# Kernel tuning notes

Hardware: AMD Instinct MI355X
Metric: run time of the kernel (lower is better)

Reference implementation:

```python
import jax, jax.numpy as jnp
import numpy as np


def _patch_indices():
    # 36 positions (6x6 grid), each gathering a 3x3 window of 6-channel squares
    # from the flattened 385-vector: index = x*48 + y*6 + c
    idx = []
    for i in range(36):
        x, y = i // 6, i % 6
        rows = []
        for ox in range(3):
            for oy in range(3):
                base = (x + ox) * 48 + (y + oy) * 6
                rows.extend(range(base, base + 6))
        idx.append(rows)
    return jnp.asarray(np.array(idx, dtype=np.int32))  # [36, 54]


_IDX = _patch_indices()


def _crelu(v):
    return jnp.clip(v, -1.0, 1.0)


def setup_inputs() -> dict:
    key = jax.random.key(0)
    ks = jax.random.split(key, 13)
    B = 131072
    inp = jax.random.normal(ks[0], (B, 385), dtype=jnp.float32)
    s = 0.2  # small init scale
    # sight stack: 54 -> 8 -> 8 -> 1  (stored as [in, out])
    W1 = jax.random.normal(ks[1], (54, 8), jnp.float32) * s
    b1 = jax.random.normal(ks[2], (8,), jnp.float32) * s
    W2 = jax.random.normal(ks[3], (8, 8), jnp.float32) * s
    b2 = jax.random.normal(ks[4], (8,), jnp.float32) * s
    W3 = jax.random.normal(ks[5], (8, 1), jnp.float32) * s
    b3 = jax.random.normal(ks[6], (1,), jnp.float32) * s
    # evaluation stack: 37 -> 16 -> 16 -> 1
    E1 = jax.random.normal(ks[7], (37, 16), jnp.float32) * s
    c1 = jax.random.normal(ks[8], (16,), jnp.float32) * s
    E2 = jax.random.normal(ks[9], (16, 16), jnp.float32) * s
    c2 = jax.random.normal(ks[10], (16,), jnp.float32) * s
    E3 = jax.random.normal(ks[11], (16, 1), jnp.float32) * s
    c3 = jax.random.normal(ks[12], (1,), jnp.float32) * s
    return {"inp": inp, "W1": W1, "b1": b1, "W2": W2, "b2": b2,
            "W3": W3, "b3": b3, "E1": E1, "c1": c1, "E2": E2, "c2": c2,
            "E3": E3, "c3": c3}


def reference(inp, W1, b1, W2, b2, W3, b3, E1, c1, E2, c2, E3, c3):
    # inp: [B, 385]
    patches = inp[:, _IDX]                       # [B, 36, 54] windowed gather
    h = _crelu(jnp.einsum('bpf,fo->bpo', patches, W1) + b1)   # [B, 36, 8]
    h = _crelu(jnp.einsum('bpf,fo->bpo', h, W2) + b2)         # [B, 36, 8]
    v = _crelu(jnp.einsum('bpf,fo->bpo', h, W3) + b3)[..., 0]  # [B, 36]
    vision = jnp.concatenate([v, inp[:, 384:385]], axis=1)    # [B, 37]
    g = _crelu(vision @ E1 + c1)                 # [B, 16]
    g = _crelu(g @ E2 + c2)                      # [B, 16]
    out = _crelu(g @ E3 + c3)                    # [B, 1]
    return out
```

## Files before the change

kernel.cpp:

```cpp
#include <hip/hip_runtime.h>

typedef __attribute__((ext_vector_type(8))) short short8;
typedef __attribute__((ext_vector_type(4))) float float4v;

__device__ __forceinline__ float crelu(float v) {
    return fminf(1.0f, fmaxf(-1.0f, v));
}
__device__ __forceinline__ uint f2bf_u(float v) {
    uint u = __float_as_uint(v);
    u += 0x7fffu + ((u >> 16) & 1u);
    return u >> 16;
}
__device__ __forceinline__ ushort f2bf(float v) { return (ushort)f2bf_u(v); }
__device__ __forceinline__ float bf2f_lo(uint u) { return __uint_as_float(u << 16); }
__device__ __forceinline__ float bf2f_hi(uint u) { return __uint_as_float(u & 0xffff0000u); }
__device__ __forceinline__ uint cvt_pk_bf16(float a, float b) {
    uint r;
    asm("v_cvt_pk_bf16_f32 %0, %1, %2" : "=v"(r) : "v"(a), "v"(b));
    return r;
}

#define ROW 385
#define BT  16

#define SLAB_BYTES 6656
#define E1T_OFF 960
#define E2T_OFF 3776
#define E1T_LD  44

__global__ __launch_bounds__(256, 6)
void lila_wave(const float* __restrict__ inp,
               const float* __restrict__ W1, const float* __restrict__ b1,
               const float* __restrict__ W2, const float* __restrict__ b2,
               const float* __restrict__ W3, const float* __restrict__ b3,
               const float* __restrict__ E1, const float* __restrict__ c1,
               const float* __restrict__ E2, const float* __restrict__ c2,
               const float* __restrict__ E3, const float* __restrict__ c3,
               float* __restrict__ out)
{
    __shared__ __align__(16) char slab_all[4 * SLAB_BYTES];

    const int tid  = threadIdx.x;
    const int lane = tid & 63;
    const int wv   = tid >> 6;
    const int quad = lane >> 4;
    const int nn   = lane & 15;
    const int m0   = quad * 8;

    char*   slab  = slab_all + wv * SLAB_BYTES;
    ushort* board = (ushort*)slab;
    ushort* hbuf  = (ushort*)(slab + 4352);
    float*  vis   = (float*)slab;
    float*  g1    = (float*)(slab + 640);
    float*  e1t   = (float*)(slab + E1T_OFF);
    ushort* e2t   = (ushort*)(slab + E2T_OFF);

    const long long b0w = (long long)blockIdx.x * BT + wv * 4;

    short8 bfr[3];
    #pragma unroll
    for (int r = 0; r < 3; ++r) {
        #pragma unroll
        for (int j = 0; j < 8; ++j) {
            int k = m0 + j, oy = k >> 3, c = k & 7;
            float w = (oy < 3 && c < 6 && nn < 8)
                    ? W1[(r * 18 + oy * 6 + c) * 8 + nn] : 0.0f;
            bfr[r][j] = (short)f2bf(w);
        }
    }
    const float bias1 = (nn < 8) ? b1[nn] : 0.0f;

    const int r   = lane >> 4;
    const int c16 = lane & 15;
    const float* gr = inp + (b0w + r) * ROW;

    if (c16 < 4) {
        uint4 z = {0u, 0u, 0u, 0u};
        *(uint4*)(board + r * 544 + 512 + c16 * 8) = z;
    }
    #pragma unroll
    for (int u = 0; u < 4; ++u) {
        int cell = c16 + 16 * u;
        int g = cell * 6;
        float4 q0 = *(const float4*)(gr + g);
        float2 q1 = *(const float2*)(gr + g + 4);
        uint4 pk;
        pk.x = cvt_pk_bf16(q0.x, q0.y);
        pk.y = cvt_pk_bf16(q0.z, q0.w);
        pk.z = cvt_pk_bf16(q1.x, q1.y);
        pk.w = 0u;
        *(uint4*)(board + r * 544 + cell * 8) = pk;
    }
    const float cen = gr[384];

    asm volatile("" ::: "memory");

    #pragma unroll 3
    for (int t = 0; t < 9; ++t) {
        int ltask = t * 16 + nn;
        uint lb = (uint)ltask / 36u;
        uint p  = (uint)ltask - 36u * lb;
        uint x  = p / 6u;
        uint y  = p - 6u * x;
        const ushort* base = board + lb * 544 + x * 64 + 8 * y + m0;
        union { uint4 u; short8 s; } a0, a1, a2;
        a0.u = *(const uint4*)(base);
        a1.u = *(const uint4*)(base + 64);
        a2.u = *(const uint4*)(base + 128);
        float4v acc = { bias1, bias1, bias1, bias1 };
        acc = __builtin_amdgcn_mfma_f32_16x16x32_bf16(a0.s, bfr[0], acc, 0, 0, 0);
        acc = __builtin_amdgcn_mfma_f32_16x16x32_bf16(a1.s, bfr[1], acc, 0, 0, 0);
        acc = __builtin_amdgcn_mfma_f32_16x16x32_bf16(a2.s, bfr[2], acc, 0, 0, 0);
        if (nn < 8) {
            uint w01 = cvt_pk_bf16(crelu(acc[0]), crelu(acc[1]));
            uint w23 = cvt_pk_bf16(crelu(acc[2]), crelu(acc[3]));
            ushort* hb = hbuf + (t * 16 + quad * 4) * 8 + nn;
            hb[0]  = (ushort)w01;
            hb[8]  = (ushort)(w01 >> 16);
            hb[16] = (ushort)w23;
            hb[24] = (ushort)(w23 >> 16);
        }
    }

    asm volatile("" ::: "memory");

    {
        float e1g[10];
        #pragma unroll
        for (int k = 0; k < 9; ++k) e1g[k] = E1[lane + 64 * k];
        if (lane < 16) e1g[9] = E1[lane + 576];
        float e2g[4];
        #pragma unroll
        for (int k = 0; k < 4; ++k) e2g[k] = E2[lane + 64 * k];

        #pragma unroll
        for (int k = 0; k < 9; ++k) e1t[nn * E1T_LD + r + 4 * k] = e1g[k];
        if (lane < 16) e1t[nn * E1T_LD + 36] = e1g[9];
        #pragma unroll
        for (int k = 0; k < 4; ++k) e2t[nn * 16 + r + 4 * k] = f2bf(e2g[k]);
    }
    const float c1v = c1[nn];
    const float c2v = c2[nn];
    const float e3v = E3[nn];

    asm volatile("" ::: "memory");

    {
        short8 w2fh, w2fl;
        const int colq = nn - quad * 8;
        #pragma unroll
        for (int j = 0; j < 8; ++j) {
            float w = (quad < 2 && colq >= 0 && colq < 8) ? W2[j * 8 + colq] : 0.0f;
            uint hb = f2bf_u(w);
            float wr = w - __uint_as_float(hb << 16);
            w2fh[j] = (short)hb;
            w2fl[j] = (short)f2bf(wr);
        }
        const float b2v = b2[nn & 7];
        const float w3v = W3[nn & 7];
        const float b3v = b3[0];

        #pragma unroll
        for (int t = 0; t < 5; ++t) {
            union { uint4 u; short8 s; } av;
            av.u.x = 0u; av.u.y = 0u; av.u.z = 0u; av.u.w = 0u;
            int tsk = t * 16 + nn + (quad ? 80 : 0);
            if (quad < 2 && (t < 4 || quad == 0))
                av.u = *(const uint4*)(hbuf + tsk * 8);
            float4v acc = { b2v, b2v, b2v, b2v };
            acc = __builtin_amdgcn_mfma_f32_16x16x32_bf16(av.s, w2fh, acc, 0, 0, 0);
            acc = __builtin_amdgcn_mfma_f32_16x16x32_bf16(av.s, w2fl, acc, 0, 0, 0);
            float vsum[4];
            #pragma unroll
            for (int i = 0; i < 4; ++i) {
                float vv = crelu(acc[i]) * w3v;
                vv += __shfl_xor(vv, 1);
                vv += __shfl_xor(vv, 2);
                vv += __shfl_xor(vv, 4);
                vsum[i] = vv;
            }
            const bool isA = (nn == 0);
            if ((nn & 7) == 0 && (isA || t < 4)) {
                int task = (isA ? 0 : 80) + t * 16 + quad * 4;
                uint lb = (uint)task / 36u;
                uint p  = (uint)task - 36u * lb;
                float4 o4;
                o4.x = crelu(vsum[0] + b3v);
                o4.y = crelu(vsum[1] + b3v);
                o4.z = crelu(vsum[2] + b3v);
                o4.w = crelu(vsum[3] + b3v);
                *(float4*)(vis + lb * 40 + p) = o4;
            }
        }
    }

    asm volatile("" ::: "memory");

    {
        const int o = nn;
        float a = c1v;
        #pragma unroll
        for (int fi = 0; fi < 9; ++fi) {
            float4 vv = *(const float4*)(vis + r * 40 + fi * 4);
            float4 ev = *(const float4*)(e1t + o * E1T_LD + fi * 4);
            a = fmaf(vv.x, ev.x, a);
            a = fmaf(vv.y, ev.y, a);
            a = fmaf(vv.z, ev.z, a);
            a = fmaf(vv.w, ev.w, a);
        }
        a = fmaf(cen, e1t[o * E1T_LD + 36], a);
        g1[r * 20 + o] = crelu(a);

        asm volatile("" ::: "memory");

        uint4 e2a = *(const uint4*)(e2t + o * 16);
        uint4 e2b = *(const uint4*)(e2t + o * 16 + 8);
        float a2 = c2v;
        #pragma unroll
        for (int fi = 0; fi < 4; ++fi) {
            float4 gv = *(const float4*)(g1 + r * 20 + fi * 4);
            uint w01 = (fi < 2) ? (fi == 0 ? e2a.x : e2a.z) : (fi == 2 ? e2b.x : e2b.z);
            uint w23 = (fi < 2) ? (fi == 0 ? e2a.y : e2a.w) : (fi == 2 ? e2b.y : e2b.w);
            a2 = fmaf(gv.x, bf2f_lo(w01), a2);
            a2 = fmaf(gv.y, bf2f_hi(w01), a2);
            a2 = fmaf(gv.z, bf2f_lo(w23), a2);
            a2 = fmaf(gv.w, bf2f_hi(w23), a2);
        }
        float tv = crelu(a2) * e3v;
        tv += __shfl_xor(tv, 1);
        tv += __shfl_xor(tv, 2);
        tv += __shfl_xor(tv, 4);
        tv += __shfl_xor(tv, 8);
        if (o == 0) out[b0w + r] = crelu(tv + c3[0]);
    }
}

extern "C" void kernel_launch(void* const* d_in, const int* in_sizes, int n_in,
                              void* d_out, int out_size, void* d_ws, size_t ws_size,
                              hipStream_t stream)
{
    const float* inp = (const float*)d_in[0];
    const float* W1  = (const float*)d_in[1];
    const float* b1  = (const float*)d_in[2];
    const float* W2  = (const float*)d_in[3];
    const float* b2  = (const float*)d_in[4];
    const float* W3  = (const float*)d_in[5];
    const float* b3  = (const float*)d_in[6];
    const float* E1  = (const float*)d_in[7];
    const float* c1  = (const float*)d_in[8];
    const float* E2  = (const float*)d_in[9];
    const float* c2  = (const float*)d_in[10];
    const float* E3  = (const float*)d_in[11];
    const float* c3  = (const float*)d_in[12];
    float* out = (float*)d_out;

    int B = in_sizes[0] / ROW;
    int grid = B / BT;
    lila_wave<<<grid, 256, 0, stream>>>(inp, W1, b1, W2, b2, W3, b3,
                                        E1, c1, E2, c2, E3, c3, out);
}
```

Before: 293.9 us.

## Reuse sliding-window rows in layer-1 MFMA loop and hoist weight loads

Layer 1 now walks each column of the 6x6 grid along x with a rotating three-row register window. Each step loads one new LDS row instead of three, and the per-task divide and modulo index math goes away. Positions are split into a 4-column group and a 2-column group, with the hbuf write layout adjusted to match. The W2, bias and E-weight global loads move earlier so their latency overlaps the convolution, and the E1/E2 LDS stores are deferred until after layer 2. The cost is higher register pressure and more complex indexing.

```diff
diff --git a/kernel.cpp b/kernel.cpp
--- a/kernel.cpp
+++ b/kernel.cpp
@@ -59,16 +59,35 @@
 
     short8 bfr[3];
     #pragma unroll
-    for (int r = 0; r < 3; ++r) {
+    for (int rr = 0; rr < 3; ++rr) {
         #pragma unroll
         for (int j = 0; j < 8; ++j) {
             int k = m0 + j, oy = k >> 3, c = k & 7;
             float w = (oy < 3 && c < 6 && nn < 8)
-                    ? W1[(r * 18 + oy * 6 + c) * 8 + nn] : 0.0f;
-            bfr[r][j] = (short)f2bf(w);
+                    ? W1[(rr * 18 + oy * 6 + c) * 8 + nn] : 0.0f;
+            bfr[rr][j] = (short)f2bf(w);
         }
     }
     const float bias1 = (nn < 8) ? b1[nn] : 0.0f;
+
+    short8 w2fh, w2fl;
+    {
+        const int colq = nn - quad * 8;
+        #pragma unroll
+        for (int j = 0; j < 8; ++j) {
+            float w = (quad < 2 && colq >= 0 && colq < 8) ? W2[j * 8 + colq] : 0.0f;
+            uint hb2 = f2bf_u(w);
+            float wr = w - __uint_as_float(hb2 << 16);
+            w2fh[j] = (short)hb2;
+            w2fl[j] = (short)f2bf(wr);
+        }
+    }
+    const float b2v = b2[nn & 7];
+    const float w3v = W3[nn & 7];
+    const float b3v = b3[0];
+    const float c1v = c1[nn];
+    const float c2v = c2[nn];
+    const float e3v = E3[nn];
 
     const int r   = lane >> 4;
     const int c16 = lane & 15;
@@ -95,71 +114,66 @@
 
     asm volatile("" ::: "memory");
 
-    #pragma unroll 3
-    for (int t = 0; t < 9; ++t) {
-        int ltask = t * 16 + nn;
-        uint lb = (uint)ltask / 36u;
-        uint p  = (uint)ltask - 36u * lb;
-        uint x  = p / 6u;
-        uint y  = p - 6u * x;
-        const ushort* base = board + lb * 544 + x * 64 + 8 * y + m0;
-        union { uint4 u; short8 s; } a0, a1, a2;
-        a0.u = *(const uint4*)(base);
-        a1.u = *(const uint4*)(base + 64);
-        a2.u = *(const uint4*)(base + 128);
-        float4v acc = { bias1, bias1, bias1, bias1 };
-        acc = __builtin_amdgcn_mfma_f32_16x16x32_bf16(a0.s, bfr[0], acc, 0, 0, 0);
-        acc = __builtin_amdgcn_mfma_f32_16x16x32_bf16(a1.s, bfr[1], acc, 0, 0, 0);
-        acc = __builtin_amdgcn_mfma_f32_16x16x32_bf16(a2.s, bfr[2], acc, 0, 0, 0);
-        if (nn < 8) {
-            uint w01 = cvt_pk_bf16(crelu(acc[0]), crelu(acc[1]));
-            uint w23 = cvt_pk_bf16(crelu(acc[2]), crelu(acc[3]));
-            ushort* hb = hbuf + (t * 16 + quad * 4) * 8 + nn;
-            hb[0]  = (ushort)w01;
-            hb[8]  = (ushort)(w01 >> 16);
-            hb[16] = (ushort)w23;
-            hb[24] = (ushort)(w23 >> 16);
+    {
+        const int lb0 = nn >> 2, y0 = nn & 3;
+        const ushort* base = board + lb0 * 544 + 8 * y0 + m0;
+        union { uint4 u; short8 s; } rw[3];
+        rw[0].u = *(const uint4*)(base);
+        rw[1].u = *(const uint4*)(base + 64);
+        #pragma unroll
+        for (int x = 0; x < 6; ++x) {
+            rw[(x + 2) % 3].u = *(const uint4*)(base + (x + 2) * 64);
+            float4v acc = { bias1, bias1, bias1, bias1 };
+            acc = __builtin_amdgcn_mfma_f32_16x16x32_bf16(rw[x % 3].s,       bfr[0], acc, 0, 0, 0);
+            acc = __builtin_amdgcn_mfma_f32_16x16x32_bf16(rw[(x + 1) % 3].s, bfr[1], acc, 0, 0, 0);
+            acc = __builtin_amdgcn_mfma_f32_16x16x32_bf16(rw[(x + 2) % 3].s, bfr[2], acc, 0, 0, 0);
+            if (nn < 8) {
+                uint w01 = cvt_pk_bf16(crelu(acc[0]), crelu(acc[1]));
+                uint w23 = cvt_pk_bf16(crelu(acc[2]), crelu(acc[3]));
+                ushort* hb = hbuf + (quad * 36 + x * 6) * 8 + nn;
+                hb[0]  = (ushort)w01;
+                hb[8]  = (ushort)(w01 >> 16);
+                hb[16] = (ushort)w23;
+                hb[24] = (ushort)(w23 >> 16);
+            }
+        }
+    }
+    {
+        const int lb1 = (nn >> 1) & 3, y1 = 4 + (nn & 1);
+        const ushort* base = board + lb1 * 544 + 8 * y1 + m0;
+        union { uint4 u; short8 s; } rw[3];
+        rw[0].u = *(const uint4*)(base);
+        rw[1].u = *(const uint4*)(base + 64);
+        #pragma unroll
+        for (int x = 0; x < 6; ++x) {
+            rw[(x + 2) % 3].u = *(const uint4*)(base + (x + 2) * 64);
+            float4v acc = { bias1, bias1, bias1, bias1 };
+            acc = __builtin_amdgcn_mfma_f32_16x16x32_bf16(rw[x % 3].s,       bfr[0], acc, 0, 0, 0);
+            acc = __builtin_amdgcn_mfma_f32_16x16x32_bf16(rw[(x + 1) % 3].s, bfr[1], acc, 0, 0, 0);
+            acc = __builtin_amdgcn_mfma_f32_16x16x32_bf16(rw[(x + 2) % 3].s, bfr[2], acc, 0, 0, 0);
+            if (quad < 2 && nn < 8) {
+                uint w01 = cvt_pk_bf16(crelu(acc[0]), crelu(acc[1]));
+                uint w23 = cvt_pk_bf16(crelu(acc[2]), crelu(acc[3]));
+                ushort* hb = hbuf + ((2 * quad) * 36 + x * 6 + 4) * 8 + nn;
+                hb[0]   = (ushort)w01;
+                hb[8]   = (ushort)(w01 >> 16);
+                hb[288] = (ushort)w23;
+                hb[296] = (ushort)(w23 >> 16);
+            }
         }
     }
 
     asm volatile("" ::: "memory");
 
-    {
-        float e1g[10];
-        #pragma unroll
-        for (int k = 0; k < 9; ++k) e1g[k] = E1[lane + 64 * k];
-        if (lane < 16) e1g[9] = E1[lane + 576];
-        float e2g[4];
-        #pragma unroll
-        for (int k = 0; k < 4; ++k) e2g[k] = E2[lane + 64 * k];
-
-        #pragma unroll
-        for (int k = 0; k < 9; ++k) e1t[nn * E1T_LD + r + 4 * k] = e1g[k];
-        if (lane < 16) e1t[nn * E1T_LD + 36] = e1g[9];
-        #pragma unroll
-        for (int k = 0; k < 4; ++k) e2t[nn * 16 + r + 4 * k] = f2bf(e2g[k]);
-    }
-    const float c1v = c1[nn];
-    const float c2v = c2[nn];
-    const float e3v = E3[nn];
-
-    asm volatile("" ::: "memory");
-
-    {
-        short8 w2fh, w2fl;
-        const int colq = nn - quad * 8;
-        #pragma unroll
-        for (int j = 0; j < 8; ++j) {
-            float w = (quad < 2 && colq >= 0 && colq < 8) ? W2[j * 8 + colq] : 0.0f;
-            uint hb = f2bf_u(w);
-            float wr = w - __uint_as_float(hb << 16);
-            w2fh[j] = (short)hb;
-            w2fl[j] = (short)f2bf(wr);
-        }
-        const float b2v = b2[nn & 7];
-        const float w3v = W3[nn & 7];
-        const float b3v = b3[0];
-
+    float e1g[10];
+    #pragma unroll
+    for (int k = 0; k < 9; ++k) e1g[k] = E1[lane + 64 * k];
+    if (lane < 16) e1g[9] = E1[lane + 576];
+    float e2g[4];
+    #pragma unroll
+    for (int k = 0; k < 4; ++k) e2g[k] = E2[lane + 64 * k];
+
+    {
         #pragma unroll
         for (int t = 0; t < 5; ++t) {
             union { uint4 u; short8 s; } av;
@@ -193,6 +207,12 @@
             }
         }
     }
+
+    #pragma unroll
+    for (int k = 0; k < 9; ++k) e1t[nn * E1T_LD + r + 4 * k] = e1g[k];
+    if (lane < 16) e1t[nn * E1T_LD + 36] = e1g[9];
+    #pragma unroll
+    for (int k = 0; k < 4; ++k) e2t[nn * 16 + r + 4 * k] = f2bf(e2g[k]);
 
     asm volatile("" ::: "memory");
 
```

Result: no change. 295.8 us (+0.7%).

## Process two row groups per wave with register prefetch of next group

Applied to the files above, without the earlier changes.

Each wave now handles two groups of 4 rows instead of one, and the launch grid shrinks by half. The input rows for the next group are loaded into registers while the current group's layer-1 results are consumed, then packed into the board buffer after the current group finishes. The aim is to hide global load latency behind compute and to amortise weight setup across more rows. In exchange it costs extra registers, under a launch bound that already targets 6 blocks, and it halves the block count. The E1/E2 staging into shared memory is also moved inside the loop, so it repeats for every group.

```diff
diff --git a/kernel.cpp b/kernel.cpp
--- a/kernel.cpp
+++ b/kernel.cpp
@@ -21,7 +21,7 @@
 }
 
 #define ROW 385
-#define BT  16
+#define NG  2
 
 #define SLAB_BYTES 6656
 #define E1T_OFF 960
@@ -46,6 +46,8 @@
     const int quad = lane >> 4;
     const int nn   = lane & 15;
     const int m0   = quad * 8;
+    const int r    = lane >> 4;
+    const int c16  = lane & 15;
 
     char*   slab  = slab_all + wv * SLAB_BYTES;
     ushort* board = (ushort*)slab;
@@ -55,183 +57,222 @@
     float*  e1t   = (float*)(slab + E1T_OFF);
     ushort* e2t   = (ushort*)(slab + E2T_OFF);
 
-    const long long b0w = (long long)blockIdx.x * BT + wv * 4;
+    const long long b0w = (long long)blockIdx.x * (4 * NG * 4) + (long long)wv * (4 * NG);
 
     short8 bfr[3];
     #pragma unroll
-    for (int r = 0; r < 3; ++r) {
+    for (int rr = 0; rr < 3; ++rr) {
         #pragma unroll
         for (int j = 0; j < 8; ++j) {
             int k = m0 + j, oy = k >> 3, c = k & 7;
             float w = (oy < 3 && c < 6 && nn < 8)
-                    ? W1[(r * 18 + oy * 6 + c) * 8 + nn] : 0.0f;
-            bfr[r][j] = (short)f2bf(w);
+                    ? W1[(rr * 18 + oy * 6 + c) * 8 + nn] : 0.0f;
+            bfr[rr][j] = (short)f2bf(w);
         }
     }
     const float bias1 = (nn < 8) ? b1[nn] : 0.0f;
 
-    const int r   = lane >> 4;
-    const int c16 = lane & 15;
-    const float* gr = inp + (b0w + r) * ROW;
-
-    if (c16 < 4) {
-        uint4 z = {0u, 0u, 0u, 0u};
-        *(uint4*)(board + r * 544 + 512 + c16 * 8) = z;
-    }
-    #pragma unroll
-    for (int u = 0; u < 4; ++u) {
-        int cell = c16 + 16 * u;
-        int g = cell * 6;
-        float4 q0 = *(const float4*)(gr + g);
-        float2 q1 = *(const float2*)(gr + g + 4);
-        uint4 pk;
-        pk.x = cvt_pk_bf16(q0.x, q0.y);
-        pk.y = cvt_pk_bf16(q0.z, q0.w);
-        pk.z = cvt_pk_bf16(q1.x, q1.y);
-        pk.w = 0u;
-        *(uint4*)(board + r * 544 + cell * 8) = pk;
-    }
-    const float cen = gr[384];
-
-    asm volatile("" ::: "memory");
-
-    #pragma unroll 3
-    for (int t = 0; t < 9; ++t) {
-        int ltask = t * 16 + nn;
-        uint lb = (uint)ltask / 36u;
-        uint p  = (uint)ltask - 36u * lb;
-        uint x  = p / 6u;
-        uint y  = p - 6u * x;
-        const ushort* base = board + lb * 544 + x * 64 + 8 * y + m0;
-        union { uint4 u; short8 s; } a0, a1, a2;
-        a0.u = *(const uint4*)(base);
-        a1.u = *(const uint4*)(base + 64);
-        a2.u = *(const uint4*)(base + 128);
-        float4v acc = { bias1, bias1, bias1, bias1 };
-        acc = __builtin_amdgcn_mfma_f32_16x16x32_bf16(a0.s, bfr[0], acc, 0, 0, 0);
-        acc = __builtin_amdgcn_mfma_f32_16x16x32_bf16(a1.s, bfr[1], acc, 0, 0, 0);
-        acc = __builtin_amdgcn_mfma_f32_16x16x32_bf16(a2.s, bfr[2], acc, 0, 0, 0);
-        if (nn < 8) {
-            uint w01 = cvt_pk_bf16(crelu(acc[0]), crelu(acc[1]));
-            uint w23 = cvt_pk_bf16(crelu(acc[2]), crelu(acc[3]));
-            ushort* hb = hbuf + (t * 16 + quad * 4) * 8 + nn;
-            hb[0]  = (ushort)w01;
-            hb[8]  = (ushort)(w01 >> 16);
-            hb[16] = (ushort)w23;
-            hb[24] = (ushort)(w23 >> 16);
-        }
-    }
-
-    asm volatile("" ::: "memory");
-
+    short8 w2fh, w2fl;
     {
-        float e1g[10];
-        #pragma unroll
-        for (int k = 0; k < 9; ++k) e1g[k] = E1[lane + 64 * k];
-        if (lane < 16) e1g[9] = E1[lane + 576];
-        float e2g[4];
-        #pragma unroll
-        for (int k = 0; k < 4; ++k) e2g[k] = E2[lane + 64 * k];
-
-        #pragma unroll
-        for (int k = 0; k < 9; ++k) e1t[nn * E1T_LD + r + 4 * k] = e1g[k];
-        if (lane < 16) e1t[nn * E1T_LD + 36] = e1g[9];
-        #pragma unroll
-        for (int k = 0; k < 4; ++k) e2t[nn * 16 + r + 4 * k] = f2bf(e2g[k]);
-    }
-    const float c1v = c1[nn];
-    const float c2v = c2[nn];
-    const float e3v = E3[nn];
-
-    asm volatile("" ::: "memory");
-
-    {
-        short8 w2fh, w2fl;
         const int colq = nn - quad * 8;
         #pragma unroll
         for (int j = 0; j < 8; ++j) {
             float w = (quad < 2 && colq >= 0 && colq < 8) ? W2[j * 8 + colq] : 0.0f;
-            uint hb = f2bf_u(w);
-            float wr = w - __uint_as_float(hb << 16);
-            w2fh[j] = (short)hb;
+            uint hb2 = f2bf_u(w);
+            float wr = w - __uint_as_float(hb2 << 16);
+            w2fh[j] = (short)hb2;
             w2fl[j] = (short)f2bf(wr);
         }
-        const float b2v = b2[nn & 7];
-        const float w3v = W3[nn & 7];
-        const float b3v = b3[0];
-
+    }
+    const float b2v = b2[nn & 7];
+    const float w3v = W3[nn & 7];
+    const float b3v = b3[0];
+    const float c1v = c1[nn];
+    const float c2v = c2[nn];
+    const float e3v = E3[nn];
+
+    float4 p4[4]; float2 p2[4]; float cen_c, cen_n = 0.0f;
+    {
+        const float* gr = inp + (b0w + r) * ROW;
         #pragma unroll
-        for (int t = 0; t < 5; ++t) {
-            union { uint4 u; short8 s; } av;
-            av.u.x = 0u; av.u.y = 0u; av.u.z = 0u; av.u.w = 0u;
-            int tsk = t * 16 + nn + (quad ? 80 : 0);
-            if (quad < 2 && (t < 4 || quad == 0))
-                av.u = *(const uint4*)(hbuf + tsk * 8);
-            float4v acc = { b2v, b2v, b2v, b2v };
-            acc = __builtin_amdgcn_mfma_f32_16x16x32_bf16(av.s, w2fh, acc, 0, 0, 0);
-            acc = __builtin_amdgcn_mfma_f32_16x16x32_bf16(av.s, w2fl, acc, 0, 0, 0);
-            float vsum[4];
-            #pragma unroll
-            for (int i = 0; i < 4; ++i) {
-                float vv = crelu(acc[i]) * w3v;
-                vv += __shfl_xor(vv, 1);
-                vv += __shfl_xor(vv, 2);
-                vv += __shfl_xor(vv, 4);
-                vsum[i] = vv;
-            }
-            const bool isA = (nn == 0);
-            if ((nn & 7) == 0 && (isA || t < 4)) {
-                int task = (isA ? 0 : 80) + t * 16 + quad * 4;
-                uint lb = (uint)task / 36u;
-                uint p  = (uint)task - 36u * lb;
-                float4 o4;
-                o4.x = crelu(vsum[0] + b3v);
-                o4.y = crelu(vsum[1] + b3v);
-                o4.z = crelu(vsum[2] + b3v);
-                o4.w = crelu(vsum[3] + b3v);
-                *(float4*)(vis + lb * 40 + p) = o4;
-            }
-        }
+        for (int u = 0; u < 4; ++u) {
+            int g6 = (c16 + 16 * u) * 6;
+            p4[u] = *(const float4*)(gr + g6);
+            p2[u] = *(const float2*)(gr + g6 + 4);
+        }
+        cen_c = gr[384];
+    }
+    if (c16 < 4) {
+        uint4 z = {0u, 0u, 0u, 0u};
+        *(uint4*)(board + r * 544 + 512 + c16 * 8) = z;
+    }
+    #pragma unroll
+    for (int u = 0; u < 4; ++u) {
+        int cell = c16 + 16 * u;
+        uint4 pk;
+        pk.x = cvt_pk_bf16(p4[u].x, p4[u].y);
+        pk.y = cvt_pk_bf16(p4[u].z, p4[u].w);
+        pk.z = cvt_pk_bf16(p2[u].x, p2[u].y);
+        pk.w = 0u;
+        *(uint4*)(board + r * 544 + cell * 8) = pk;
     }
 
     asm volatile("" ::: "memory");
 
-    {
-        const int o = nn;
-        float a = c1v;
-        #pragma unroll
-        for (int fi = 0; fi < 9; ++fi) {
-            float4 vv = *(const float4*)(vis + r * 40 + fi * 4);
-            float4 ev = *(const float4*)(e1t + o * E1T_LD + fi * 4);
-            a = fmaf(vv.x, ev.x, a);
-            a = fmaf(vv.y, ev.y, a);
-            a = fmaf(vv.z, ev.z, a);
-            a = fmaf(vv.w, ev.w, a);
-        }
-        a = fmaf(cen, e1t[o * E1T_LD + 36], a);
-        g1[r * 20 + o] = crelu(a);
+    #pragma unroll 1
+    for (int gi = 0; gi < NG; ++gi) {
+        #pragma unroll 3
+        for (int t = 0; t < 9; ++t) {
+            int ltask = t * 16 + nn;
+            uint lb = (uint)ltask / 36u;
+            uint p  = (uint)ltask - 36u * lb;
+            uint x  = p / 6u;
+            uint y  = p - 6u * x;
+            const ushort* base = board + lb * 544 + x * 64 + 8 * y + m0;
+            union { uint4 u; short8 s; } a0, a1, a2;
+            a0.u = *(const uint4*)(base);
+            a1.u = *(const uint4*)(base + 64);
+            a2.u = *(const uint4*)(base + 128);
+            float4v acc = { bias1, bias1, bias1, bias1 };
+            acc = __builtin_amdgcn_mfma_f32_16x16x32_bf16(a0.s, bfr[0], acc, 0, 0, 0);
+            acc = __builtin_amdgcn_mfma_f32_16x16x32_bf16(a1.s, bfr[1], acc, 0, 0, 0);
+            acc = __builtin_amdgcn_mfma_f32_16x16x32_bf16(a2.s, bfr[2], acc, 0, 0, 0);
+            if (nn < 8) {
+                uint w01 = cvt_pk_bf16(crelu(acc[0]), crelu(acc[1]));
+                uint w23 = cvt_pk_bf16(crelu(acc[2]), crelu(acc[3]));
+                ushort* hb = hbuf + (t * 16 + quad * 4) * 8 + nn;
+                hb[0]  = (ushort)w01;
+                hb[8]  = (ushort)(w01 >> 16);
+                hb[16] = (ushort)w23;
+                hb[24] = (ushort)(w23 >> 16);
+            }
+        }
 
         asm volatile("" ::: "memory");
 
-        uint4 e2a = *(const uint4*)(e2t + o * 16);
-        uint4 e2b = *(const uint4*)(e2t + o * 16 + 8);
-        float a2 = c2v;
-        #pragma unroll
-        for (int fi = 0; fi < 4; ++fi) {
-            float4 gv = *(const float4*)(g1 + r * 20 + fi * 4);
-            uint w01 = (fi < 2) ? (fi == 0 ? e2a.x : e2a.z) : (fi == 2 ? e2b.x : e2b.z);
-            uint w23 = (fi < 2) ? (fi == 0 ? e2a.y : e2a.w) : (fi == 2 ? e2b.y : e2b.w);
-            a2 = fmaf(gv.x, bf2f_lo(w01), a2);
-            a2 = fmaf(gv.y, bf2f_hi(w01), a2);
-            a2 = fmaf(gv.z, bf2f_lo(w23), a2);
-            a2 = fmaf(gv.w, bf2f_hi(w23), a2);
-        }
-        float tv = crelu(a2) * e3v;
-        tv += __shfl_xor(tv, 1);
-        tv += __shfl_xor(tv, 2);
-        tv += __shfl_xor(tv, 4);
-        tv += __shfl_xor(tv, 8);
-        if (o == 0) out[b0w + r] = crelu(tv + c3[0]);
+        if (gi + 1 < NG) {
+            const float* gr = inp + (b0w + (gi + 1) * 4 + r) * ROW;
+            #pragma unroll
+            for (int u = 0; u < 4; ++u) {
+                int g6 = (c16 + 16 * u) * 6;
+                p4[u] = *(const float4*)(gr + g6);
+                p2[u] = *(const float2*)(gr + g6 + 4);
+            }
+            cen_n = gr[384];
+        }
+
+        {
+            float e1g[10];
+            #pragma unroll
+            for (int k = 0; k < 9; ++k) e1g[k] = E1[lane + 64 * k];
+            if (lane < 16) e1g[9] = E1[lane + 576];
+            float e2g[4];
+            #pragma unroll
+            for (int k = 0; k < 4; ++k) e2g[k] = E2[lane + 64 * k];
+
+            #pragma unroll
+            for (int k = 0; k < 9; ++k) e1t[nn * E1T_LD + r + 4 * k] = e1g[k];
+            if (lane < 16) e1t[nn * E1T_LD + 36] = e1g[9];
+            #pragma unroll
+            for (int k = 0; k < 4; ++k) e2t[nn * 16 + r + 4 * k] = f2bf(e2g[k]);
+        }
+
+        asm volatile("" ::: "memory");
+
+        {
+            #pragma unroll
+            for (int t = 0; t < 5; ++t) {
+                union { uint4 u; short8 s; } av;
+                av.u.x = 0u; av.u.y = 0u; av.u.z = 0u; av.u.w = 0u;
+                int tsk = t * 16 + nn + (quad ? 80 : 0);
+                if (quad < 2 && (t < 4 || quad == 0))
+                    av.u = *(const uint4*)(hbuf + tsk * 8);
+                float4v acc = { b2v, b2v, b2v, b2v };
+                acc = __builtin_amdgcn_mfma_f32_16x16x32_bf16(av.s, w2fh, acc, 0, 0, 0);
+                acc = __builtin_amdgcn_mfma_f32_16x16x32_bf16(av.s, w2fl, acc, 0, 0, 0);
+                float vsum[4];
+                #pragma unroll
+                for (int i = 0; i < 4; ++i) {
+                    float vv = crelu(acc[i]) * w3v;
+                    vv += __shfl_xor(vv, 1);
+                    vv += __shfl_xor(vv, 2);
+                    vv += __shfl_xor(vv, 4);
+                    vsum[i] = vv;
+                }
+                const bool isA = (nn == 0);
+                if ((nn & 7) == 0 && (isA || t < 4)) {
+                    int task = (isA ? 0 : 80) + t * 16 + quad * 4;
+                    uint lb = (uint)task / 36u;
+                    uint p  = (uint)task - 36u * lb;
+                    float4 o4;
+                    o4.x = crelu(vsum[0] + b3v);
+                    o4.y = crelu(vsum[1] + b3v);
+                    o4.z = crelu(vsum[2] + b3v);
+                    o4.w = crelu(vsum[3] + b3v);
+                    *(float4*)(vis + lb * 40 + p) = o4;
+                }
+            }
+        }
+
+        asm volatile("" ::: "memory");
+
+        {
+            const int o = nn;
+            float a = c1v;
+            #pragma unroll
+            for (int fi = 0; fi < 9; ++fi) {
+                float4 vv = *(const float4*)(vis + r * 40 + fi * 4);
+                float4 ev = *(const float4*)(e1t + o * E1T_LD + fi * 4);
+                a = fmaf(vv.x, ev.x, a);
+                a = fmaf(vv.y, ev.y, a);
+                a = fmaf(vv.z, ev.z, a);
+                a = fmaf(vv.w, ev.w, a);
+            }
+            a = fmaf(cen_c, e1t[o * E1T_LD + 36], a);
+            g1[r * 20 + o] = crelu(a);
+
+            asm volatile("" ::: "memory");
+
+            uint4 e2a = *(const uint4*)(e2t + o * 16);
+            uint4 e2b = *(const uint4*)(e2t + o * 16 + 8);
+            float a2 = c2v;
+            #pragma unroll
+            for (int fi = 0; fi < 4; ++fi) {
+                float4 gv = *(const float4*)(g1 + r * 20 + fi * 4);
+                uint w01 = (fi < 2) ? (fi == 0 ? e2a.x : e2a.z) : (fi == 2 ? e2b.x : e2b.z);
+                uint w23 = (fi < 2) ? (fi == 0 ? e2a.y : e2a.w) : (fi == 2 ? e2b.y : e2b.w);
+                a2 = fmaf(gv.x, bf2f_lo(w01), a2);
+                a2 = fmaf(gv.y, bf2f_hi(w01), a2);
+                a2 = fmaf(gv.z, bf2f_lo(w23), a2);
+                a2 = fmaf(gv.w, bf2f_hi(w23), a2);
+            }
+            float tv = crelu(a2) * e3v;
+            tv += __shfl_xor(tv, 1);
+            tv += __shfl_xor(tv, 2);
+            tv += __shfl_xor(tv, 4);
+            tv += __shfl_xor(tv, 8);
+            if (o == 0) out[b0w + gi * 4 + r] = crelu(tv + c3[0]);
+        }
+
+        if (gi + 1 < NG) {
+            asm volatile("" ::: "memory");
+            if (c16 < 4) {
+                uint4 z = {0u, 0u, 0u, 0u};
+                *(uint4*)(board + r * 544 + 512 + c16 * 8) = z;
+            }
+            #pragma unroll
+            for (int u = 0; u < 4; ++u) {
+                int cell = c16 + 16 * u;
+                uint4 pk;
+                pk.x = cvt_pk_bf16(p4[u].x, p4[u].y);
+                pk.y = cvt_pk_bf16(p4[u].z, p4[u].w);
+                pk.z = cvt_pk_bf16(p2[u].x, p2[u].y);
+                pk.w = 0u;
+                *(uint4*)(board + r * 544 + cell * 8) = pk;
+            }
+            cen_c = cen_n;
+            asm volatile("" ::: "memory");
+        }
     }
 }
 
@@ -255,7 +296,7 @@
     float* out = (float*)d_out;
 
     int B = in_sizes[0] / ROW;
-    int grid = B / BT;
+    int grid = B / (16 * NG);
     lila_wave<<<grid, 256, 0, stream>>>(inp, W1, b1, W2, b2, W3, b3,
                                         E1, c1, E2, c2, E3, c3, out);
 }
```

Result: slower. 446.8 us (+52.0%).
